# Performance work log

Measured on AMD Instinct MI355X. Metric: run time of the kernel, lower is better.

Reference implementation:

```python
import jax, jax.numpy as jnp
import numpy as np
from jax import lax

B, C, H, W = 32, 640, 8, 64
G, HEADS, HC = 4, 8, 80
KK, STRIDE = 9, 2
GC = C // G  # n_group_channels = 160
ORF = 2.0    # offset_range_factor
LN_EPS = 1e-5


def _ref_points(h, w):
    # normalized (y, x) centers in [-1, 1], matching torch linspace(0.5, h-0.5, h)/h*2-1
    ry = (jnp.arange(h, dtype=jnp.float32) + 0.5) / h * 2.0 - 1.0
    rx = (jnp.arange(w, dtype=jnp.float32) + 0.5) / w * 2.0 - 1.0
    yy, xx = jnp.meshgrid(ry, rx, indexing='ij')
    return jnp.stack([yy, xx], axis=-1)  # [h, w, 2]


def _grid_sample(img, grid):
    # img: [N, C, Hi, Wi]; grid: [N, Hg, Wg, 2] with (x, y) in [-1, 1]
    # bilinear, align_corners=False, zero padding (torch F.grid_sample semantics)
    N, Ch, Hi, Wi = img.shape
    gx = (grid[..., 0] + 1.0) * Wi * 0.5 - 0.5
    gy = (grid[..., 1] + 1.0) * Hi * 0.5 - 0.5
    x0 = jnp.floor(gx); y0 = jnp.floor(gy)
    wx1 = gx - x0; wx0 = 1.0 - wx1
    wy1 = gy - y0; wy0 = 1.0 - wy1

    def pick(xf, yf):
        xi = xf.astype(jnp.int32); yi = yf.astype(jnp.int32)
        valid = ((xi >= 0) & (xi < Wi) & (yi >= 0) & (yi < Hi)).astype(img.dtype)
        xc = jnp.clip(xi, 0, Wi - 1); yc = jnp.clip(yi, 0, Hi - 1)
        v = jax.vmap(lambda im, yy, xx: im[:, yy, xx])(img, yc, xc)  # [N, C, Hg, Wg]
        return v * valid[:, None]

    out = (pick(x0, y0) * (wx0 * wy0)[:, None]
           + pick(x0 + 1, y0) * (wx1 * wy0)[:, None]
           + pick(x0, y0 + 1) * (wx0 * wy1)[:, None]
           + pick(x0 + 1, y0 + 1) * (wx1 * wy1)[:, None])
    return out


def _conv1x1(t, w, b):
    return jnp.einsum('bchw,oc->bohw', t, w) + b[None, :, None, None]


def _forward(x, y, off_w1, off_b1, ln_g, ln_b, off_w2, qw, qb, kw, kb, vw, vb, ow, ob, rpe):
    scale = HC ** -0.5
    # offset network input: concat(x, y) regrouped -> [B*G, 2*GC, H, W]
    q_off = jnp.concatenate([x, y], axis=1).reshape(B, G, 2 * GC, H, W).reshape(B * G, 2 * GC, H, W)
    # depthwise-ish grouped conv (groups = GC)
    o = lax.conv_general_dilated(q_off, off_w1, (STRIDE, STRIDE),
                                 [(KK // 2, KK // 2), (KK // 2, KK // 2)],
                                 dimension_numbers=('NCHW', 'OIHW', 'NCHW'),
                                 feature_group_count=GC)
    o = o + off_b1[None, :, None, None]
    # LayerNormProxy over channels
    o = o.transpose(0, 2, 3, 1)
    mu = o.mean(-1, keepdims=True)
    var = o.var(-1, keepdims=True)
    o = (o - mu) / jnp.sqrt(var + LN_EPS) * ln_g + ln_b
    o = jax.nn.gelu(o, approximate=False)
    offset = jnp.einsum('nhwc,oc->nohw', o, off_w2)  # [B*G, 2, Hk, Wk]
    Hk, Wk = offset.shape[2], offset.shape[3]
    ns = Hk * Wk
    off_range = jnp.array([1.0 / Hk, 1.0 / Wk], dtype=x.dtype).reshape(1, 2, 1, 1)
    offset = jnp.tanh(offset) * off_range * ORF
    offset = offset.transpose(0, 2, 3, 1)  # [B*G, Hk, Wk, 2] (y, x)
    ref = _ref_points(Hk, Wk)              # [Hk, Wk, 2]
    pos = offset + ref[None]               # [B*G, Hk, Wk, 2]

    q = _conv1x1(y, qw, qb)
    # deformable KV sampling: grid takes (x, y) order
    xs = _grid_sample(x.reshape(B * G, GC, H, W), pos[..., ::-1])  # [B*G, GC, Hk, Wk]
    xs = xs.reshape(B, C, 1, ns)
    k = _conv1x1(xs, kw, kb).reshape(B * HEADS, HC, ns)
    v = _conv1x1(xs, vw, vb).reshape(B * HEADS, HC, ns)
    qh = q.reshape(B * HEADS, HC, H * W)

    attn = jnp.einsum('bcm,bcn->bmn', qh, k) * scale  # [B*HEADS, HW, ns]

    # relative position bias via grid_sample on RPE table
    qg = _ref_points(H, W).reshape(H * W, 2)  # same for every batch/group
    disp = (qg[None, :, None, :] - pos.reshape(B * G, ns, 2)[:, None, :, :]) * 0.5  # [B*G, HW, ns, 2]
    rpe_b = jnp.broadcast_to(rpe[None], (B,) + rpe.shape).reshape(B * G, HEADS // G, 2 * H - 1, 2 * W - 1)
    attn_bias = _grid_sample(rpe_b, disp[..., ::-1]).reshape(B * HEADS, H * W, ns)
    attn = jax.nn.softmax(attn + attn_bias, axis=2)

    out = jnp.einsum('bmn,bcn->bcm', attn, v).reshape(B, C, H, W)
    out = _conv1x1(out, ow, ob)
    pos_out = pos.reshape(B, G, Hk, Wk, 2)
    ref_out = jnp.broadcast_to(ref[None, None], (B, G, Hk, Wk, 2))
    return out, pos_out, ref_out


def setup_inputs() -> dict:
    key = jax.random.key(0)
    ks = jax.random.split(key, 10)
    r = lambda k, s, std=0.02: jax.random.normal(k, s, dtype=jnp.float32) * std
    return {
        'x': jax.random.normal(ks[0], (B, C, H, W), dtype=jnp.float32),
        'y': jax.random.normal(ks[1], (B, C, H, W), dtype=jnp.float32),
        'off_w1': r(ks[2], (2 * GC, 2, KK, KK)),
        'off_b1': jnp.zeros((2 * GC,), jnp.float32),
        'ln_g': jnp.ones((2 * GC,), jnp.float32),
        'ln_b': jnp.zeros((2 * GC,), jnp.float32),
        'off_w2': r(ks[3], (2, 2 * GC)),
        'qw': r(ks[4], (C, C)), 'qb': jnp.zeros((C,), jnp.float32),
        'kw': r(ks[5], (C, C)), 'kb': jnp.zeros((C,), jnp.float32),
        'vw': r(ks[6], (C, C)), 'vb': jnp.zeros((C,), jnp.float32),
        'ow': r(ks[7], (C, C)), 'ob': jnp.zeros((C,), jnp.float32),
        'rpe': r(ks[8], (HEADS, 2 * H - 1, 2 * W - 1), 0.01),
    }


def reference(x, y, off_w1, off_b1, ln_g, ln_b, off_w2, qw, qb, kw, kb, vw, vb, ow, ob, rpe):
    return _forward(x, y, off_w1, off_b1, ln_g, ln_b, off_w2, qw, qb, kw, kb, vw, vb, ow, ob, rpe)
```

## Files before the change

kernel.cpp:

```cpp
#include <hip/hip_runtime.h>

#define DI static __device__ __forceinline__

typedef __attribute__((ext_vector_type(8))) short s8v;
typedef __attribute__((ext_vector_type(4))) short s4v;
typedef __attribute__((ext_vector_type(4))) float f4v;

DI short f2b(float x) {
  unsigned u = __builtin_bit_cast(unsigned, x);
  u = (u + 0x7fffu + ((u >> 16) & 1u)) >> 16;
  return (short)u;
}
DI float b2f(short s) {
  unsigned u = ((unsigned)(unsigned short)s) << 16;
  return __builtin_bit_cast(float, u);
}
DI f4v mfma16(s8v a, s8v b, f4v c) {
  return __builtin_amdgcn_mfma_f32_16x16x32_bf16(a, b, c, 0, 0, 0);
}
DI void gload16(const short* g, short* l) {
  __builtin_amdgcn_global_load_lds(
      (const __attribute__((address_space(1))) unsigned*)g,
      (__attribute__((address_space(3))) unsigned*)l, 16, 0, 0);
}

__global__ __launch_bounds__(256) void cvtw4_k(
    const float* __restrict__ s0, const float* __restrict__ s1,
    const float* __restrict__ s2, const float* __restrict__ s3,
    short* __restrict__ d0, short* __restrict__ d1,
    short* __restrict__ d2, short* __restrict__ d3) {
  int w = blockIdx.y;
  const float* s = (w == 0) ? s0 : (w == 1) ? s1 : (w == 2) ? s2 : s3;
  short* d = (w == 0) ? d0 : (w == 1) ? d1 : (w == 2) ? d2 : d3;
  int i = blockIdx.x * 256 + threadIdx.x;
  d[i] = f2b(s[i]);
}

__global__ __launch_bounds__(256) void conv_off_k(
    const float* __restrict__ x, const float* __restrict__ y,
    const float* __restrict__ w1, const float* __restrict__ b1,
    float* __restrict__ co)
{
  __shared__ float si[8 * 8 * 84 + 84];
  const int cc = blockIdx.x;
  const int n  = blockIdx.y;
  const int b = n >> 2, g = n & 3;
  const int c0 = cc * 8;
  const float* src = (g < 2 ? x : y) + ((size_t)b * 640 + (g & 1) * 320 + c0) * 512;
  const int tid = threadIdx.x;
  float* const zb = &si[8 * 8 * 84];

  for (int i = tid; i < 512; i += 256) {
    int chrow = i >> 3, t = i & 7;
    int par = t & 1, which = t >> 1;
    int idx = (which < 2) ? which : 32 + which;
    si[chrow * 84 + par * 42 + idx] = 0.f;
  }
  for (int i = tid; i < 84; i += 256) zb[i] = 0.f;
  for (int i = tid; i < 8 * 512; i += 256) {
    int ch = i >> 9, idx = i & 511;
    int r = idx >> 6, c = idx & 63;
    int pc = c + 4;
    si[(ch * 8 + r) * 84 + (pc & 1) * 42 + (pc >> 1)] = src[(size_t)ch * 512 + idx];
  }
  __syncthreads();

  const int lane = tid & 63, wvi = tid >> 6;
  const int cl = lane & 15, rg = lane >> 4;
  const int ocs = __builtin_amdgcn_readfirstlane(c0 + 2 * wvi);
  const float* wbase = w1 + (size_t)ocs * 162;
  float a00 = 0.f, a01 = 0.f, a10 = 0.f, a11 = 0.f;
#pragma unroll
  for (int ic = 0; ic < 2; ++ic) {
    const float* chb = &si[(2 * wvi + ic) * 8 * 84];
#pragma unroll
    for (int kh = 0; kh < 9; ++kh) {
      const int row = 2 * rg + kh - 4;
      const float* rp = ((unsigned)row < 8u) ? (chb + row * 84) : zb;
      float ev[6], ov[5];
#pragma unroll
      for (int t = 0; t < 6; ++t) ev[t] = rp[2 * cl + t];
#pragma unroll
      for (int t = 0; t < 5; ++t) ov[t] = rp[42 + 2 * cl + t];
      const float* wv0 = wbase + ic * 81 + kh * 9;
      const float* wv1 = wv0 + 162;
#pragma unroll
      for (int kw = 0; kw < 9; ++kw) {
        float w0 = wv0[kw], w1v = wv1[kw];
        int j = kw >> 1;
        float v0 = (kw & 1) ? ov[j] : ev[j];
        float v1 = (kw & 1) ? ov[j + 1] : ev[j + 1];
        a00 = fmaf(v0, w0, a00);
        a01 = fmaf(v1, w0, a01);
        a10 = fmaf(v0, w1v, a10);
        a11 = fmaf(v1, w1v, a11);
      }
    }
  }
  const float bv0 = b1[ocs], bv1 = b1[ocs + 1];
  const int s0 = rg * 32 + 2 * cl;
  float2 vA = {a00 + bv0, a10 + bv1};
  float2 vB = {a01 + bv0, a11 + bv1};
  *(float2*)&co[((size_t)n * 128 + s0) * 320 + ocs] = vA;
  *(float2*)&co[((size_t)n * 128 + s0 + 1) * 320 + ocs] = vB;
}

__global__ __launch_bounds__(256) void ln_proj_k(
    const float* __restrict__ co, const float* __restrict__ lng,
    const float* __restrict__ lnb, const float* __restrict__ w2,
    float* __restrict__ pos, float* __restrict__ pos_out, float* __restrict__ ref_out)
{
  const int n = blockIdx.y;
  const int wvi = threadIdx.x >> 6, lane = threadIdx.x & 63;
  const int s = blockIdx.x * 4 + wvi;
  const float* cp = co + ((size_t)n * 128 + s) * 320;
  float v[5], gw[5], gb[5], p0[5], p1[5];
#pragma unroll
  for (int t = 0; t < 5; ++t) {
    int ch = lane + 64 * t;
    v[t] = cp[ch]; gw[t] = lng[ch]; gb[t] = lnb[ch];
    p0[t] = w2[ch]; p1[t] = w2[320 + ch];
  }
  float s1 = 0.f, s2 = 0.f;
#pragma unroll
  for (int t = 0; t < 5; ++t) { s1 += v[t]; s2 += v[t] * v[t]; }
#pragma unroll
  for (int o = 32; o; o >>= 1) { s1 += __shfl_xor(s1, o); s2 += __shfl_xor(s2, o); }
  float mu = s1 * (1.f / 320.f);
  float var = s2 * (1.f / 320.f) - mu * mu;
  float rstd = rsqrtf(var + 1e-5f);
  float d0 = 0.f, d1 = 0.f;
#pragma unroll
  for (int t = 0; t < 5; ++t) {
    float xn = (v[t] - mu) * rstd * gw[t] + gb[t];
    float ge = 0.5f * xn * (1.f + erff(xn * 0.70710678118654752f));
    d0 = fmaf(ge, p0[t], d0);
    d1 = fmaf(ge, p1[t], d1);
  }
#pragma unroll
  for (int o = 32; o; o >>= 1) { d0 += __shfl_xor(d0, o); d1 += __shfl_xor(d1, o); }
  if (lane == 0) {
    float oy = tanhf(d0) * 0.5f;
    float ox = tanhf(d1) * 0.0625f;
    int hk = s >> 5, wk = s & 31;
    float ry = ((float)hk + 0.5f) * 0.5f - 1.f;
    float rx = ((float)wk + 0.5f) * 0.0625f - 1.f;
    float py = oy + ry, px = ox + rx;
    size_t o2 = ((size_t)n * 128 + s) * 2;
    pos[o2] = py;     pos[o2 + 1] = px;
    pos_out[o2] = py; pos_out[o2 + 1] = px;
    ref_out[o2] = ry; ref_out[o2 + 1] = rx;
  }
}

__global__ __launch_bounds__(256) void transpose_k(
    const float* __restrict__ x, const float* __restrict__ y,
    short* __restrict__ xt, short* __restrict__ yt) {
  __shared__ float tile[32][33];
  const int ct = blockIdx.x, st = blockIdx.y, z = blockIdx.z;
  const int b = z & 31;
  const float* srcm = (z < 32) ? x : y;
  short* dstm = (z < 32) ? xt : yt;
  const int tx = threadIdx.x, ty = threadIdx.y;
  const float* src = srcm + ((size_t)b * 640 + ct * 32) * 512 + st * 32;
#pragma unroll
  for (int k2 = 0; k2 < 4; ++k2)
    tile[ty + 8 * k2][tx] = src[(size_t)(ty + 8 * k2) * 512 + tx];
  __syncthreads();
  short* dst = dstm + ((size_t)b * 512 + st * 32) * 640 + ct * 32;
#pragma unroll
  for (int k2 = 0; k2 < 4; ++k2)
    dst[(size_t)(ty + 8 * k2) * 640 + tx] = f2b(tile[tx][ty + 8 * k2]);
}

__global__ __launch_bounds__(256) void sample_k(const short* __restrict__ xt,
                                                const float* __restrict__ pos,
                                                short* __restrict__ xs) {
  const int sc = blockIdx.x, bg = blockIdx.y;
  const int b = bg >> 2, g = bg & 3;
  const int t = threadIdx.x;
  const int s = sc * 8 + (t >> 5);
  const int ci = t & 31;
  size_t p2 = ((size_t)bg * 128 + s) * 2;
  float py = pos[p2], px = pos[p2 + 1];
  float gx = (px + 1.f) * 32.f - 0.5f;
  float gy = (py + 1.f) * 4.f - 0.5f;
  float fx = floorf(gx), fy = floorf(gy);
  int x0 = (int)fx, y0 = (int)fy;
  float wx1 = gx - fx, wx0 = 1.f - wx1;
  float wy1 = gy - fy, wy0 = 1.f - wy1;
  int xx[2] = {x0, x0 + 1}, yy[2] = {y0, y0 + 1};
  float wxs[2] = {wx0, wx1}, wys[2] = {wy0, wy1};
  const short* basep = xt + (size_t)b * 512 * 640 + (size_t)g * 160;
  short* outp = xs + ((size_t)(b * 128 + s)) * 640 + g * 160;
#pragma unroll
  for (int kk = 0; kk < 5; ++kk) {
    int c = kk * 32 + ci;
    float acc = 0.f;
#pragma unroll
    for (int ty = 0; ty < 2; ++ty) {
      int yv = yy[ty];
      bool vy = (yv >= 0) & (yv < 8);
      int yc = min(max(yv, 0), 7);
#pragma unroll
      for (int tx = 0; tx < 2; ++tx) {
        int xv = xx[tx];
        bool vv = vy & (xv >= 0) & (xv < 64);
        int xc = min(max(xv, 0), 63);
        float val = b2f(basep[((size_t)yc * 64 + xc) * 640 + c]);
        acc += wys[ty] * wxs[tx] * (vv ? val : 0.f);
      }
    }
    outp[c] = f2b(acc);
  }
}

template <bool BIASN, bool OUTF32>
__global__ __launch_bounds__(256) void gemm128_k(
    const short* __restrict__ W, long long wStride,
    const short* __restrict__ X, long long xStride,
    const float* __restrict__ bias, void* __restrict__ Out,
    int M, int K, int N)
{
  __shared__ short wa[2][128 * 32];
  __shared__ short xb[2][128 * 32];
  const int m0 = blockIdx.x * 128, n0 = blockIdx.y * 128;
  const int bz = blockIdx.z;
  const short* Wp = W + (size_t)bz * wStride + (size_t)m0 * K;
  const short* Xp = X + (size_t)bz * xStride + (size_t)n0 * K;
  const int tid = threadIdx.x;
  const int lane = tid & 63;
  const int wvi = __builtin_amdgcn_readfirstlane(tid >> 6);
  const int wr = wvi >> 1, wc = wvi & 1, lr = lane & 15, lg = lane >> 4;

  const int r0 = (wvi * 16) + (lane >> 2);
  const int cb = (lane & 3) * 8;
  const short* wg0 = Wp + (size_t)r0 * K + cb;
  const short* wg1 = Wp + (size_t)(r0 + 64) * K + cb;
  const short* xg0 = Xp + (size_t)r0 * K + cb;
  const short* xg1 = Xp + (size_t)(r0 + 64) * K + cb;

  f4v acc[4][4];
#pragma unroll
  for (int i = 0; i < 4; ++i)
#pragma unroll
    for (int j = 0; j < 4; ++j) acc[i][j] = (f4v)0.0f;

  const int nk = K >> 5;
  gload16(wg0, &wa[0][wvi * 512]);
  gload16(wg1, &wa[0][(4 + wvi) * 512]);
  gload16(xg0, &xb[0][wvi * 512]);
  gload16(xg1, &xb[0][(4 + wvi) * 512]);
  __syncthreads();

  int cur = 0;
  for (int ks = 0; ks < nk; ++ks) {
    if (ks + 1 < nk) {
      const int ko = (ks + 1) * 32;
      const int nb = cur ^ 1;
      gload16(wg0 + ko, &wa[nb][wvi * 512]);
      gload16(wg1 + ko, &wa[nb][(4 + wvi) * 512]);
      gload16(xg0 + ko, &xb[nb][wvi * 512]);
      gload16(xg1 + ko, &xb[nb][(4 + wvi) * 512]);
    }
    s8v av[4], bv[4];
#pragma unroll
    for (int i = 0; i < 4; ++i)
      av[i] = *(const s8v*)&wa[cur][(wr * 64 + i * 16 + lr) * 32 + lg * 8];
#pragma unroll
    for (int j = 0; j < 4; ++j)
      bv[j] = *(const s8v*)&xb[cur][(wc * 64 + j * 16 + lr) * 32 + lg * 8];
#pragma unroll
    for (int i = 0; i < 4; ++i)
#pragma unroll
      for (int j = 0; j < 4; ++j)
        acc[i][j] = mfma16(av[i], bv[j], acc[i][j]);
    __syncthreads();
    cur ^= 1;
  }

#pragma unroll
  for (int i = 0; i < 4; ++i)
#pragma unroll
    for (int j = 0; j < 4; ++j)
#pragma unroll
      for (int r = 0; r < 4; ++r) {
        int m_g = m0 + wr * 64 + i * 16 + lg * 4 + r;
        int n_g = n0 + wc * 64 + j * 16 + lr;
        float val = acc[i][j][r] + (BIASN ? bias[n_g] : bias[m_g]);
        size_t oidx = (size_t)bz * M * N + (size_t)m_g * N + n_g;
        if (OUTF32) ((float*)Out)[oidx] = val;
        else        ((short*)Out)[oidx] = f2b(val);
      }
}

__global__ __launch_bounds__(256) void qkpv_k(
    const short* __restrict__ q_t, const short* __restrict__ k_t,
    const short* __restrict__ v_, const float* __restrict__ pos,
    const float* __restrict__ rpe, short* __restrict__ ao_t)
{
  __shared__ short kT[128 * 104];
  __shared__ short vT[80 * 136];
  __shared__ short pT[64 * 136];
  __shared__ float rpeL[21 * 132];
  __shared__ float pynL[128], pxnL[128];
  const int bh = blockIdx.x, mh = blockIdx.y;
  const int b = bh >> 3, h = bh & 7, g = h >> 1;
  const int bg = b * 4 + g;
  const int tid = threadIdx.x;
  const int lane = tid & 63, wvi = tid >> 6;
  const int lr = lane & 15, lg = lane >> 4;

  for (int i = tid; i < 21 * 132; i += 256) rpeL[i] = 0.f;
  if (tid < 128) {
    float py = pos[(size_t)bg * 256 + tid * 2];
    float px = pos[(size_t)bg * 256 + tid * 2 + 1];
    pynL[tid] = 10.0f - py * 3.75f;
    pxnL[tid] = 66.0f - px * 31.75f;
  }
  const short* kp = k_t + (size_t)b * 128 * 640 + h * 80;
  for (int idx = tid; idx < 1280; idx += 256) {
    int row = idx / 10, cb = idx - row * 10;
    *(s8v*)&kT[row * 104 + cb * 8] = *(const s8v*)&kp[(size_t)row * 640 + cb * 8];
  }
  for (int idx = tid; idx < 384; idx += 256) {
    int row = idx / 3, cb = idx - row * 3;
    *(s8v*)&kT[row * 104 + 80 + cb * 8] = (s8v)(short)0;
  }
  const short* vp = v_ + ((size_t)b * 640 + h * 80) * 128;
  for (int idx = tid; idx < 1280; idx += 256) {
    int row = idx >> 4, cb = idx & 15;
    *(s8v*)&vT[row * 136 + cb * 8] = *(const s8v*)&vp[(size_t)row * 128 + cb * 8];
  }
  __syncthreads();
  for (int i = tid; i < 15 * 127; i += 256) {
    int r = i / 127, c = i - r * 127;
    rpeL[(r + 3) * 132 + (c + 3)] = rpe[(size_t)h * (15 * 127) + i];
  }
  __syncthreads();

  const float scale = 0.11180339887498949f;
  const short* qbase = q_t + ((size_t)b * 512 + mh * 256 + wvi * 16) * 640 + h * 80;
  short* aobase = ao_t + ((size_t)b * 512 + mh * 256 + wvi * 16) * 640 + h * 80;

  for (int mt = 0; mt < 4; ++mt) {
    const int m0 = mh * 256 + mt * 64;
    const short* qp = qbase + (size_t)mt * 64 * 640;

    f4v acc[8];
#pragma unroll
    for (int j = 0; j < 8; ++j) acc[j] = (f4v)0.0f;
#pragma unroll
    for (int ks = 0; ks < 3; ++ks) {
      const int ch = (ks * 4 + lg) * 8;
      s8v qv = (ch < 80) ? *(const s8v*)&qp[(size_t)lr * 640 + ch] : (s8v)(short)0;
#pragma unroll
      for (int j = 0; j < 8; ++j) {
        s8v kv = *(const s8v*)&kT[(j * 16 + lr) * 104 + ch];
        acc[j] = mfma16(kv, qv, acc[j]);
      }
    }

    const int m_g = m0 + wvi * 16 + lr;
    const float gyc = ((float)(m_g >> 6) * 0.25f + (0.125f - 1.f)) * 3.75f;
    const float gxc = ((float)(m_g & 63) * 0.03125f + (0.015625f - 1.f)) * 31.75f;
    float mx = -1e30f;
#pragma unroll
    for (int j = 0; j < 8; ++j) {
      f4v pyv = *(const f4v*)&pynL[j * 16 + lg * 4];
      f4v pxv = *(const f4v*)&pxnL[j * 16 + lg * 4];
#pragma unroll
      for (int r = 0; r < 4; ++r) {
        float gy = gyc + pyv[r], gx = gxc + pxv[r];
        float fy = floorf(gy), fx = floorf(gx);
        int iy = (int)fy, ix = (int)fx;
        float wy = gy - fy, wx = gx - fx;
        const float* t = &rpeL[iy * 132 + ix];
        float t00 = t[0], t01 = t[1], t10 = t[132], t11 = t[133];
        float top = fmaf(wx, t01 - t00, t00);
        float bot = fmaf(wx, t11 - t10, t10);
        float bias = fmaf(wy, bot - top, top);
        float sv = fmaf(acc[j][r], scale, bias);
        acc[j][r] = sv;
        mx = fmaxf(mx, sv);
      }
    }
    mx = fmaxf(mx, __shfl_xor(mx, 16));
    mx = fmaxf(mx, __shfl_xor(mx, 32));
    float sm = 0.f;
#pragma unroll
    for (int j = 0; j < 8; ++j)
#pragma unroll
      for (int r = 0; r < 4; ++r) {
        float e = __expf(acc[j][r] - mx);
        acc[j][r] = e;
        sm += e;
      }
    sm += __shfl_xor(sm, 16);
    sm += __shfl_xor(sm, 32);
    const float inv = 1.f / sm;
#pragma unroll
    for (int j = 0; j < 8; ++j) {
      s4v pk;
#pragma unroll
      for (int r = 0; r < 4; ++r) pk[r] = f2b(acc[j][r] * inv);
      *(s4v*)&pT[(wvi * 16 + lr) * 136 + j * 16 + lg * 4] = pk;
    }

    f4v pacc[5];
#pragma unroll
    for (int t = 0; t < 5; ++t) pacc[t] = (f4v)0.0f;
#pragma unroll
    for (int ks = 0; ks < 4; ++ks) {
      s8v pa = *(const s8v*)&pT[(wvi * 16 + lr) * 136 + ks * 32 + lg * 8];
#pragma unroll
      for (int ct = 0; ct < 5; ++ct) {
        s8v vb = *(const s8v*)&vT[(ct * 16 + lr) * 136 + ks * 32 + lg * 8];
        pacc[ct] = mfma16(pa, vb, pacc[ct]);
      }
    }
    short* aop = aobase + (size_t)mt * 64 * 640;
#pragma unroll
    for (int ct = 0; ct < 5; ++ct)
#pragma unroll
      for (int r = 0; r < 4; ++r)
        aop[(size_t)(lg * 4 + r) * 640 + ct * 16 + lr] = f2b(pacc[ct][r]);
  }
}

extern "C" void kernel_launch(void* const* d_in, const int* in_sizes, int n_in,
                              void* d_out, int out_size, void* d_ws, size_t ws_size,
                              hipStream_t stream) {
  (void)in_sizes; (void)n_in; (void)out_size; (void)ws_size;
  const float* x   = (const float*)d_in[0];
  const float* y   = (const float*)d_in[1];
  const float* w1  = (const float*)d_in[2];
  const float* b1  = (const float*)d_in[3];
  const float* lng = (const float*)d_in[4];
  const float* lnb = (const float*)d_in[5];
  const float* w2  = (const float*)d_in[6];
  const float* qw  = (const float*)d_in[7];
  const float* qb  = (const float*)d_in[8];
  const float* kw  = (const float*)d_in[9];
  const float* kb  = (const float*)d_in[10];
  const float* vw  = (const float*)d_in[11];
  const float* vb  = (const float*)d_in[12];
  const float* ow  = (const float*)d_in[13];
  const float* ob  = (const float*)d_in[14];
  const float* rpe = (const float*)d_in[15];
  float* out = (float*)d_out;
  float* pos_out = out + 10485760;
  float* ref_out = out + 10518528;

  char* base = (char*)d_ws;
  size_t off = 0;
  auto take = [&](size_t bytes) {
    char* pch = base + off;
    off = (off + bytes + 255) & ~(size_t)255;
    return pch;
  };
  float* pos   = (float*)take(131072);
  short* x_t   = (short*)take(20971520);
  short* y_t   = (short*)take(20971520);
  short* q_t   = (short*)take(20971520);
  short* qw_bf = (short*)take(819200);
  short* kw_bf = (short*)take(819200);
  short* vw_bf = (short*)take(819200);
  short* ow_bf = (short*)take(819200);
  short* xs_bf = (short*)take(5242880);
  short* k_t   = (short*)take(5242880);
  short* v_bf  = (short*)take(5242880);
  char*  regB  = take(20971520);
  float* co    = (float*)regB;
  short* ao_t  = (short*)regB;

  transpose_k<<<dim3(20, 16, 64), dim3(32, 8), 0, stream>>>(x, y, x_t, y_t);
  cvtw4_k<<<dim3(1600, 4), 256, 0, stream>>>(qw, kw, vw, ow, qw_bf, kw_bf, vw_bf, ow_bf);

  conv_off_k<<<dim3(40, 128), 256, 0, stream>>>(x, y, w1, b1, co);
  ln_proj_k<<<dim3(32, 128), 256, 0, stream>>>(co, lng, lnb, w2, pos, pos_out, ref_out);

  sample_k<<<dim3(16, 128), 256, 0, stream>>>(x_t, pos, xs_bf);

  gemm128_k<true,  false><<<dim3(4, 5, 32), 256, 0, stream>>>(y_t, 512LL * 640, qw_bf, 0LL, qb, q_t, 512, 640, 640);
  gemm128_k<true,  false><<<dim3(1, 5, 32), 256, 0, stream>>>(xs_bf, 128LL * 640, kw_bf, 0LL, kb, k_t, 128, 640, 640);
  gemm128_k<false, false><<<dim3(5, 1, 32), 256, 0, stream>>>(vw_bf, 0LL, xs_bf, 128LL * 640, vb, v_bf, 640, 640, 128);

  qkpv_k<<<dim3(256, 2), 256, 0, stream>>>(q_t, k_t, v_bf, pos, rpe, ao_t);

  gemm128_k<false, true><<<dim3(5, 4, 32), 256, 0, stream>>>(ow_bf, 0LL, ao_t, 512LL * 640, ob, out, 640, 640, 512);
}
```

Measured before the change: 208.2 us.

## Merge independent kernels into horizontally fused launches to cut launch count

```diff
diff --git a/kernel.cpp b/kernel.cpp
--- a/kernel.cpp
+++ b/kernel.cpp
@@ -24,85 +24,176 @@
       (__attribute__((address_space(3))) unsigned*)l, 16, 0, 0);
 }
 
-__global__ __launch_bounds__(256) void cvtw4_k(
-    const float* __restrict__ s0, const float* __restrict__ s1,
-    const float* __restrict__ s2, const float* __restrict__ s3,
-    short* __restrict__ d0, short* __restrict__ d1,
-    short* __restrict__ d2, short* __restrict__ d3) {
-  int w = blockIdx.y;
-  const float* s = (w == 0) ? s0 : (w == 1) ? s1 : (w == 2) ? s2 : s3;
-  short* d = (w == 0) ? d0 : (w == 1) ? d1 : (w == 2) ? d2 : d3;
-  int i = blockIdx.x * 256 + threadIdx.x;
-  d[i] = f2b(s[i]);
-}
-
-__global__ __launch_bounds__(256) void conv_off_k(
+DI void gemm128_dev(const short* Wp, const short* Xp, const float* bias,
+                    void* Out, int M, int K, int N, int m0, int n0, size_t obase,
+                    bool biasn, bool outf32, short* wa, short* xb)
+{
+  const int tid = threadIdx.x;
+  const int lane = tid & 63;
+  const int wvi = __builtin_amdgcn_readfirstlane(tid >> 6);
+  const int wr = wvi >> 1, wc = wvi & 1, lr = lane & 15, lg = lane >> 4;
+
+  const int r0 = (wvi * 16) + (lane >> 2);
+  const int cb = (lane & 3) * 8;
+  const short* wg0 = Wp + (size_t)r0 * K + cb;
+  const short* wg1 = Wp + (size_t)(r0 + 64) * K + cb;
+  const short* xg0 = Xp + (size_t)r0 * K + cb;
+  const short* xg1 = Xp + (size_t)(r0 + 64) * K + cb;
+
+  f4v acc[4][4];
+#pragma unroll
+  for (int i = 0; i < 4; ++i)
+#pragma unroll
+    for (int j = 0; j < 4; ++j) acc[i][j] = (f4v)0.0f;
+
+  const int nk = K >> 5;
+  gload16(wg0, &wa[wvi * 512]);
+  gload16(wg1, &wa[(4 + wvi) * 512]);
+  gload16(xg0, &xb[wvi * 512]);
+  gload16(xg1, &xb[(4 + wvi) * 512]);
+  __syncthreads();
+
+  int cur = 0;
+  for (int ks = 0; ks < nk; ++ks) {
+    if (ks + 1 < nk) {
+      const int ko = (ks + 1) * 32;
+      const int nb = cur ^ 1;
+      gload16(wg0 + ko, &wa[nb * 4096 + wvi * 512]);
+      gload16(wg1 + ko, &wa[nb * 4096 + (4 + wvi) * 512]);
+      gload16(xg0 + ko, &xb[nb * 4096 + wvi * 512]);
+      gload16(xg1 + ko, &xb[nb * 4096 + (4 + wvi) * 512]);
+    }
+    s8v av[4], bv[4];
+#pragma unroll
+    for (int i = 0; i < 4; ++i)
+      av[i] = *(const s8v*)&wa[cur * 4096 + (wr * 64 + i * 16 + lr) * 32 + lg * 8];
+#pragma unroll
+    for (int j = 0; j < 4; ++j)
+      bv[j] = *(const s8v*)&xb[cur * 4096 + (wc * 64 + j * 16 + lr) * 32 + lg * 8];
+#pragma unroll
+    for (int i = 0; i < 4; ++i)
+#pragma unroll
+      for (int j = 0; j < 4; ++j)
+        acc[i][j] = mfma16(av[i], bv[j], acc[i][j]);
+    __syncthreads();
+    cur ^= 1;
+  }
+
+#pragma unroll
+  for (int i = 0; i < 4; ++i)
+#pragma unroll
+    for (int j = 0; j < 4; ++j)
+#pragma unroll
+      for (int r = 0; r < 4; ++r) {
+        int m_g = m0 + wr * 64 + i * 16 + lg * 4 + r;
+        int n_g = n0 + wc * 64 + j * 16 + lr;
+        float val = acc[i][j][r] + (biasn ? bias[n_g] : bias[m_g]);
+        size_t oidx = obase + (size_t)m_g * N + n_g;
+        if (outf32) ((float*)Out)[oidx] = val;
+        else        ((short*)Out)[oidx] = f2b(val);
+      }
+}
+
+__global__ __launch_bounds__(256) void prep_k(
     const float* __restrict__ x, const float* __restrict__ y,
     const float* __restrict__ w1, const float* __restrict__ b1,
-    float* __restrict__ co)
-{
-  __shared__ float si[8 * 8 * 84 + 84];
-  const int cc = blockIdx.x;
-  const int n  = blockIdx.y;
-  const int b = n >> 2, g = n & 3;
-  const int c0 = cc * 8;
-  const float* src = (g < 2 ? x : y) + ((size_t)b * 640 + (g & 1) * 320 + c0) * 512;
+    float* __restrict__ co, short* __restrict__ xt, short* __restrict__ yt,
+    const float* __restrict__ qw, const float* __restrict__ kw,
+    const float* __restrict__ vw, const float* __restrict__ ow,
+    short* __restrict__ qwb, short* __restrict__ kwb,
+    short* __restrict__ vwb, short* __restrict__ owb)
+{
+  __shared__ float smemF[8 * 8 * 84 + 84];
+  const int bid = blockIdx.x;
   const int tid = threadIdx.x;
-  float* const zb = &si[8 * 8 * 84];
-
-  for (int i = tid; i < 512; i += 256) {
-    int chrow = i >> 3, t = i & 7;
-    int par = t & 1, which = t >> 1;
-    int idx = (which < 2) ? which : 32 + which;
-    si[chrow * 84 + par * 42 + idx] = 0.f;
-  }
-  for (int i = tid; i < 84; i += 256) zb[i] = 0.f;
-  for (int i = tid; i < 8 * 512; i += 256) {
-    int ch = i >> 9, idx = i & 511;
-    int r = idx >> 6, c = idx & 63;
-    int pc = c + 4;
-    si[(ch * 8 + r) * 84 + (pc & 1) * 42 + (pc >> 1)] = src[(size_t)ch * 512 + idx];
-  }
-  __syncthreads();
-
-  const int lane = tid & 63, wvi = tid >> 6;
-  const int cl = lane & 15, rg = lane >> 4;
-  const int ocs = __builtin_amdgcn_readfirstlane(c0 + 2 * wvi);
-  const float* wbase = w1 + (size_t)ocs * 162;
-  float a00 = 0.f, a01 = 0.f, a10 = 0.f, a11 = 0.f;
-#pragma unroll
-  for (int ic = 0; ic < 2; ++ic) {
-    const float* chb = &si[(2 * wvi + ic) * 8 * 84];
-#pragma unroll
-    for (int kh = 0; kh < 9; ++kh) {
-      const int row = 2 * rg + kh - 4;
-      const float* rp = ((unsigned)row < 8u) ? (chb + row * 84) : zb;
-      float ev[6], ov[5];
-#pragma unroll
-      for (int t = 0; t < 6; ++t) ev[t] = rp[2 * cl + t];
-#pragma unroll
-      for (int t = 0; t < 5; ++t) ov[t] = rp[42 + 2 * cl + t];
-      const float* wv0 = wbase + ic * 81 + kh * 9;
-      const float* wv1 = wv0 + 162;
-#pragma unroll
-      for (int kw = 0; kw < 9; ++kw) {
-        float w0 = wv0[kw], w1v = wv1[kw];
-        int j = kw >> 1;
-        float v0 = (kw & 1) ? ov[j] : ev[j];
-        float v1 = (kw & 1) ? ov[j + 1] : ev[j + 1];
-        a00 = fmaf(v0, w0, a00);
-        a01 = fmaf(v1, w0, a01);
-        a10 = fmaf(v0, w1v, a10);
-        a11 = fmaf(v1, w1v, a11);
-      }
-    }
-  }
-  const float bv0 = b1[ocs], bv1 = b1[ocs + 1];
-  const int s0 = rg * 32 + 2 * cl;
-  float2 vA = {a00 + bv0, a10 + bv1};
-  float2 vB = {a01 + bv0, a11 + bv1};
-  *(float2*)&co[((size_t)n * 128 + s0) * 320 + ocs] = vA;
-  *(float2*)&co[((size_t)n * 128 + s0 + 1) * 320 + ocs] = vB;
+
+  if (bid < 5120) {
+    const int cc = bid % 40;
+    const int n  = bid / 40;
+    const int b = n >> 2, g = n & 3;
+    const int c0 = cc * 8;
+    const float* src = (g < 2 ? x : y) + ((size_t)b * 640 + (g & 1) * 320 + c0) * 512;
+    float* const si = smemF;
+    float* const zb = &si[8 * 8 * 84];
+
+    for (int i = tid; i < 512; i += 256) {
+      int chrow = i >> 3, t = i & 7;
+      int par = t & 1, which = t >> 1;
+      int idx = (which < 2) ? which : 32 + which;
+      si[chrow * 84 + par * 42 + idx] = 0.f;
+    }
+    for (int i = tid; i < 84; i += 256) zb[i] = 0.f;
+    for (int i = tid; i < 8 * 512; i += 256) {
+      int ch = i >> 9, idx = i & 511;
+      int r = idx >> 6, c = idx & 63;
+      int pc = c + 4;
+      si[(ch * 8 + r) * 84 + (pc & 1) * 42 + (pc >> 1)] = src[(size_t)ch * 512 + idx];
+    }
+    __syncthreads();
+
+    const int lane = tid & 63, wvi = tid >> 6;
+    const int cl = lane & 15, rg = lane >> 4;
+    const int ocs = __builtin_amdgcn_readfirstlane(c0 + 2 * wvi);
+    const float* wbase = w1 + (size_t)ocs * 162;
+    float a00 = 0.f, a01 = 0.f, a10 = 0.f, a11 = 0.f;
+#pragma unroll
+    for (int ic = 0; ic < 2; ++ic) {
+      const float* chb = &si[(2 * wvi + ic) * 8 * 84];
+#pragma unroll
+      for (int kh = 0; kh < 9; ++kh) {
+        const int row = 2 * rg + kh - 4;
+        const float* rp = ((unsigned)row < 8u) ? (chb + row * 84) : zb;
+        float ev[6], ov[5];
+#pragma unroll
+        for (int t = 0; t < 6; ++t) ev[t] = rp[2 * cl + t];
+#pragma unroll
+        for (int t = 0; t < 5; ++t) ov[t] = rp[42 + 2 * cl + t];
+        const float* wv0 = wbase + ic * 81 + kh * 9;
+        const float* wv1 = wv0 + 162;
+#pragma unroll
+        for (int kw2 = 0; kw2 < 9; ++kw2) {
+          float w0 = wv0[kw2], w1v = wv1[kw2];
+          int j = kw2 >> 1;
+          float v0 = (kw2 & 1) ? ov[j] : ev[j];
+          float v1 = (kw2 & 1) ? ov[j + 1] : ev[j + 1];
+          a00 = fmaf(v0, w0, a00);
+          a01 = fmaf(v1, w0, a01);
+          a10 = fmaf(v0, w1v, a10);
+          a11 = fmaf(v1, w1v, a11);
+        }
+      }
+    }
+    const float bv0 = b1[ocs], bv1 = b1[ocs + 1];
+    const int s0 = rg * 32 + 2 * cl;
+    float2 vA = {a00 + bv0, a10 + bv1};
+    float2 vB = {a01 + bv0, a11 + bv1};
+    *(float2*)&co[((size_t)n * 128 + s0) * 320 + ocs] = vA;
+    *(float2*)&co[((size_t)n * 128 + s0 + 1) * 320 + ocs] = vB;
+  } else if (bid < 25600) {
+    const int t = bid - 5120;
+    const int ct = t % 20, st = (t / 20) % 16, z = t / 320;
+    const int b = z & 31;
+    const float* srcm = (z < 32) ? x : y;
+    short* dstm = (z < 32) ? xt : yt;
+    const int tx = tid & 31, ty = tid >> 5;
+    float* tile = smemF;
+    const float* src = srcm + ((size_t)b * 640 + ct * 32) * 512 + st * 32;
+#pragma unroll
+    for (int k2 = 0; k2 < 4; ++k2)
+      tile[(ty + 8 * k2) * 33 + tx] = src[(size_t)(ty + 8 * k2) * 512 + tx];
+    __syncthreads();
+    short* dst = dstm + ((size_t)b * 512 + st * 32) * 640 + ct * 32;
+#pragma unroll
+    for (int k2 = 0; k2 < 4; ++k2)
+      dst[(size_t)(ty + 8 * k2) * 640 + tx] = f2b(tile[tx * 33 + ty + 8 * k2]);
+  } else {
+    const int t = bid - 25600;
+    const int w = t / 1600;
+    const int i = (t % 1600) * 256 + tid;
+    const float* s = (w == 0) ? qw : (w == 1) ? kw : (w == 2) ? vw : ow;
+    short* d = (w == 0) ? qwb : (w == 1) ? kwb : (w == 2) ? vwb : owb;
+    d[i] = f2b(s[i]);
+  }
 }
 
 __global__ __launch_bounds__(256) void ln_proj_k(
@@ -153,32 +244,29 @@
   }
 }
 
-__global__ __launch_bounds__(256) void transpose_k(
-    const float* __restrict__ x, const float* __restrict__ y,
-    short* __restrict__ xt, short* __restrict__ yt) {
-  __shared__ float tile[32][33];
-  const int ct = blockIdx.x, st = blockIdx.y, z = blockIdx.z;
-  const int b = z & 31;
-  const float* srcm = (z < 32) ? x : y;
-  short* dstm = (z < 32) ? xt : yt;
-  const int tx = threadIdx.x, ty = threadIdx.y;
-  const float* src = srcm + ((size_t)b * 640 + ct * 32) * 512 + st * 32;
-#pragma unroll
-  for (int k2 = 0; k2 < 4; ++k2)
-    tile[ty + 8 * k2][tx] = src[(size_t)(ty + 8 * k2) * 512 + tx];
-  __syncthreads();
-  short* dst = dstm + ((size_t)b * 512 + st * 32) * 640 + ct * 32;
-#pragma unroll
-  for (int k2 = 0; k2 < 4; ++k2)
-    dst[(size_t)(ty + 8 * k2) * 640 + tx] = f2b(tile[tx][ty + 8 * k2]);
-}
-
-__global__ __launch_bounds__(256) void sample_k(const short* __restrict__ xt,
-                                                const float* __restrict__ pos,
-                                                short* __restrict__ xs) {
-  const int sc = blockIdx.x, bg = blockIdx.y;
+__global__ __launch_bounds__(256) void sampq_k(
+    const short* __restrict__ y_t, const short* __restrict__ qw_bf,
+    const float* __restrict__ qb, short* __restrict__ q_t,
+    const short* __restrict__ xt, const float* __restrict__ pos,
+    short* __restrict__ xs)
+{
+  __shared__ short wa[2 * 4096];
+  __shared__ short xb[2 * 4096];
+  const int bid = blockIdx.x;
+  const int t = threadIdx.x;
+
+  if (bid < 640) {
+    const int mx = bid % 4, ny = (bid / 4) % 5, bz = bid / 20;
+    const int m0 = mx * 128, n0 = ny * 128;
+    const short* Wp = y_t + (size_t)bz * 512 * 640 + (size_t)m0 * 640;
+    const short* Xp = qw_bf + (size_t)n0 * 640;
+    gemm128_dev(Wp, Xp, qb, q_t, 512, 640, 640, m0, n0, (size_t)bz * 512 * 640,
+                true, false, wa, xb);
+    return;
+  }
+  const int tt = bid - 640;
+  const int sc = tt % 16, bg = tt / 16;
   const int b = bg >> 2, g = bg & 3;
-  const int t = threadIdx.x;
   const int s = sc * 8 + (t >> 5);
   const int ci = t & 31;
   size_t p2 = ((size_t)bg * 128 + s) * 2;
@@ -215,83 +303,45 @@
   }
 }
 
-template <bool BIASN, bool OUTF32>
-__global__ __launch_bounds__(256) void gemm128_k(
-    const short* __restrict__ W, long long wStride,
-    const short* __restrict__ X, long long xStride,
-    const float* __restrict__ bias, void* __restrict__ Out,
-    int M, int K, int N)
-{
-  __shared__ short wa[2][128 * 32];
-  __shared__ short xb[2][128 * 32];
-  const int m0 = blockIdx.x * 128, n0 = blockIdx.y * 128;
-  const int bz = blockIdx.z;
-  const short* Wp = W + (size_t)bz * wStride + (size_t)m0 * K;
-  const short* Xp = X + (size_t)bz * xStride + (size_t)n0 * K;
-  const int tid = threadIdx.x;
-  const int lane = tid & 63;
-  const int wvi = __builtin_amdgcn_readfirstlane(tid >> 6);
-  const int wr = wvi >> 1, wc = wvi & 1, lr = lane & 15, lg = lane >> 4;
-
-  const int r0 = (wvi * 16) + (lane >> 2);
-  const int cb = (lane & 3) * 8;
-  const short* wg0 = Wp + (size_t)r0 * K + cb;
-  const short* wg1 = Wp + (size_t)(r0 + 64) * K + cb;
-  const short* xg0 = Xp + (size_t)r0 * K + cb;
-  const short* xg1 = Xp + (size_t)(r0 + 64) * K + cb;
-
-  f4v acc[4][4];
-#pragma unroll
-  for (int i = 0; i < 4; ++i)
-#pragma unroll
-    for (int j = 0; j < 4; ++j) acc[i][j] = (f4v)0.0f;
-
-  const int nk = K >> 5;
-  gload16(wg0, &wa[0][wvi * 512]);
-  gload16(wg1, &wa[0][(4 + wvi) * 512]);
-  gload16(xg0, &xb[0][wvi * 512]);
-  gload16(xg1, &xb[0][(4 + wvi) * 512]);
-  __syncthreads();
-
-  int cur = 0;
-  for (int ks = 0; ks < nk; ++ks) {
-    if (ks + 1 < nk) {
-      const int ko = (ks + 1) * 32;
-      const int nb = cur ^ 1;
-      gload16(wg0 + ko, &wa[nb][wvi * 512]);
-      gload16(wg1 + ko, &wa[nb][(4 + wvi) * 512]);
-      gload16(xg0 + ko, &xb[nb][wvi * 512]);
-      gload16(xg1 + ko, &xb[nb][(4 + wvi) * 512]);
-    }
-    s8v av[4], bv[4];
-#pragma unroll
-    for (int i = 0; i < 4; ++i)
-      av[i] = *(const s8v*)&wa[cur][(wr * 64 + i * 16 + lr) * 32 + lg * 8];
-#pragma unroll
-    for (int j = 0; j < 4; ++j)
-      bv[j] = *(const s8v*)&xb[cur][(wc * 64 + j * 16 + lr) * 32 + lg * 8];
-#pragma unroll
-    for (int i = 0; i < 4; ++i)
-#pragma unroll
-      for (int j = 0; j < 4; ++j)
-        acc[i][j] = mfma16(av[i], bv[j], acc[i][j]);
-    __syncthreads();
-    cur ^= 1;
-  }
-
-#pragma unroll
-  for (int i = 0; i < 4; ++i)
-#pragma unroll
-    for (int j = 0; j < 4; ++j)
-#pragma unroll
-      for (int r = 0; r < 4; ++r) {
-        int m_g = m0 + wr * 64 + i * 16 + lg * 4 + r;
-        int n_g = n0 + wc * 64 + j * 16 + lr;
-        float val = acc[i][j][r] + (BIASN ? bias[n_g] : bias[m_g]);
-        size_t oidx = (size_t)bz * M * N + (size_t)m_g * N + n_g;
-        if (OUTF32) ((float*)Out)[oidx] = val;
-        else        ((short*)Out)[oidx] = f2b(val);
-      }
+__global__ __launch_bounds__(256) void kv_k(
+    const short* __restrict__ xs_bf, const short* __restrict__ kw_bf,
+    const float* __restrict__ kb, short* __restrict__ k_t,
+    const short* __restrict__ vw_bf, const float* __restrict__ vb,
+    short* __restrict__ v_bf)
+{
+  __shared__ short wa[2 * 4096];
+  __shared__ short xb[2 * 4096];
+  const int bid = blockIdx.x;
+  if (bid < 160) {
+    const int ny = bid % 5, bz = bid / 5;
+    const int n0 = ny * 128;
+    const short* Wp = xs_bf + (size_t)bz * 128 * 640;
+    const short* Xp = kw_bf + (size_t)n0 * 640;
+    gemm128_dev(Wp, Xp, kb, k_t, 128, 640, 640, 0, n0, (size_t)bz * 128 * 640,
+                true, false, wa, xb);
+  } else {
+    const int t2 = bid - 160;
+    const int mx = t2 % 5, bz = t2 / 5;
+    const int m0 = mx * 128;
+    const short* Wp = vw_bf + (size_t)m0 * 640;
+    const short* Xp = xs_bf + (size_t)bz * 128 * 640;
+    gemm128_dev(Wp, Xp, vb, v_bf, 640, 640, 128, m0, 0, (size_t)bz * 640 * 128,
+                false, false, wa, xb);
+  }
+}
+
+__global__ __launch_bounds__(256) void gemmO_k(
+    const short* __restrict__ ow_bf, const short* __restrict__ ao_t,
+    const float* __restrict__ ob, float* __restrict__ out)
+{
+  __shared__ short wa[2 * 4096];
+  __shared__ short xb[2 * 4096];
+  const int mx = blockIdx.x, ny = blockIdx.y, bz = blockIdx.z;
+  const int m0 = mx * 128, n0 = ny * 128;
+  const short* Wp = ow_bf + (size_t)m0 * 640;
+  const short* Xp = ao_t + (size_t)bz * 512 * 640 + (size_t)n0 * 640;
+  gemm128_dev(Wp, Xp, ob, out, 640, 640, 512, m0, n0, (size_t)bz * 640 * 512,
+              false, true, wa, xb);
 }
 
 __global__ __launch_bounds__(256) void qkpv_k(
@@ -474,19 +524,16 @@
   float* co    = (float*)regB;
   short* ao_t  = (short*)regB;
 
-  transpose_k<<<dim3(20, 16, 64), dim3(32, 8), 0, stream>>>(x, y, x_t, y_t);
-  cvtw4_k<<<dim3(1600, 4), 256, 0, stream>>>(qw, kw, vw, ow, qw_bf, kw_bf, vw_bf, ow_bf);
-
-  conv_off_k<<<dim3(40, 128), 256, 0, stream>>>(x, y, w1, b1, co);
+  prep_k<<<32000, 256, 0, stream>>>(x, y, w1, b1, co, x_t, y_t,
+                                    qw, kw, vw, ow, qw_bf, kw_bf, vw_bf, ow_bf);
+
   ln_proj_k<<<dim3(32, 128), 256, 0, stream>>>(co, lng, lnb, w2, pos, pos_out, ref_out);
 
-  sample_k<<<dim3(16, 128), 256, 0, stream>>>(x_t, pos, xs_bf);
-
-  gemm128_k<true,  false><<<dim3(4, 5, 32), 256, 0, stream>>>(y_t, 512LL * 640, qw_bf, 0LL, qb, q_t, 512, 640, 640);
-  gemm128_k<true,  false><<<dim3(1, 5, 32), 256, 0, stream>>>(xs_bf, 128LL * 640, kw_bf, 0LL, kb, k_t, 128, 640, 640);
-  gemm128_k<false, false><<<dim3(5, 1, 32), 256, 0, stream>>>(vw_bf, 0LL, xs_bf, 128LL * 640, vb, v_bf, 640, 640, 128);
+  sampq_k<<<2688, 256, 0, stream>>>(y_t, qw_bf, qb, q_t, x_t, pos, xs_bf);
+
+  kv_k<<<320, 256, 0, stream>>>(xs_bf, kw_bf, kb, k_t, vw_bf, vb, v_bf);
 
   qkpv_k<<<dim3(256, 2), 256, 0, stream>>>(q_t, k_t, v_bf, pos, rpe, ao_t);
 
-  gemm128_k<false, true><<<dim3(5, 4, 32), 256, 0, stream>>>(ow_bf, 0LL, ao_t, 512LL * 640, ob, out, 640, 640, 512);
-}
+  gemmO_k<<<dim3(5, 4, 32), 256, 0, stream>>>(ow_bf, ao_t, ob, out);
+}
```

Result: faster. 175.1 us (median of 2 runs) (-15.9%).
